# Kernel optimization log

Measured on AMD Instinct MI355X. Metric: run time of the kernel, lower is better.

## Reference

```python
import jax, jax.numpy as jnp
import numpy as np

B, T, C, H, W, NC = 128, 32, 512, 8, 32, 6625
HH = C // 2  # per-direction LSTM hidden


def setup_inputs() -> dict:
    key = jax.random.key(0)
    ks = jax.random.split(key, 20)
    u = lambda k, shape, n: jax.random.uniform(k, shape, jnp.float32, -1.0 / np.sqrt(n), 1.0 / np.sqrt(n))
    return dict(
        feature=jax.random.normal(ks[0], (B, C, H, W), jnp.float32),
        attention_map=jax.random.uniform(ks[1], (B, T, H, W), jnp.float32) + 1e-3,
        text=jax.random.randint(ks[2], (B, T), 0, NC),
        text_length=jnp.full((B,), T, dtype=jnp.int32),
        char_embeddings=jax.random.normal(ks[3], (NC, C), jnp.float32),
        lstm_w_ih_f=u(ks[4], (4 * HH, C), HH),
        lstm_w_hh_f=u(ks[5], (4 * HH, HH), HH),
        lstm_b_ih_f=u(ks[6], (4 * HH,), HH),
        lstm_b_hh_f=u(ks[7], (4 * HH,), HH),
        lstm_w_ih_b=u(ks[8], (4 * HH, C), HH),
        lstm_w_hh_b=u(ks[9], (4 * HH, HH), HH),
        lstm_b_ih_b=u(ks[10], (4 * HH,), HH),
        lstm_b_hh_b=u(ks[11], (4 * HH,), HH),
        gru_w_ih=u(ks[12], (3 * C, 2 * C), C),
        gru_w_hh=u(ks[13], (3 * C, C), C),
        gru_b_ih=u(ks[14], (3 * C,), C),
        gru_b_hh=u(ks[15], (3 * C,), C),
        gen_w=u(ks[16], (NC, C), C),
        gen_b=u(ks[17], (NC,), C),
    )


def _lstm_dir(xs, w_ih, w_hh, b_ih, b_hh):
    # xs: [T, B, C] -> hs: [T, B, HH]; PyTorch gate order i, f, g, o
    b = xs.shape[1]
    hh = w_hh.shape[1]
    def step(carry, xt):
        h, c = carry
        g = xt @ w_ih.T + h @ w_hh.T + (b_ih + b_hh)
        i, f, gg, o = jnp.split(g, 4, axis=-1)
        c = jax.nn.sigmoid(f) * c + jax.nn.sigmoid(i) * jnp.tanh(gg)
        h = jax.nn.sigmoid(o) * jnp.tanh(c)
        return (h, c), h
    h0 = jnp.zeros((b, hh), xs.dtype)
    _, hs = jax.lax.scan(step, (h0, h0), xs)
    return hs


def reference(feature, attention_map, text, text_length, char_embeddings,
              lstm_w_ih_f, lstm_w_hh_f, lstm_b_ih_f, lstm_b_hh_f,
              lstm_w_ih_b, lstm_w_hh_b, lstm_b_ih_b, lstm_b_hh_b,
              gru_w_ih, gru_w_hh, gru_b_ih, gru_b_hh, gen_w, gen_b):
    b, c, h, w = feature.shape
    t = attention_map.shape[1]
    # normalize attention over spatial dims, attention-pool features: [T, B, C]
    att = attention_map / attention_map.sum(axis=(2, 3), keepdims=True)
    cseq = jnp.einsum('bchw,bthw->tbc', feature, att)
    # bidirectional LSTM (dropout is identity in eval mode)
    hs_f = _lstm_dir(cseq, lstm_w_ih_f, lstm_w_hh_f, lstm_b_ih_f, lstm_b_hh_f)
    hs_b = _lstm_dir(cseq[::-1], lstm_w_ih_b, lstm_w_hh_b, lstm_b_ih_b, lstm_b_hh_b)[::-1]
    cseq = jnp.concatenate([hs_f, hs_b], axis=-1)  # [T, B, C]
    # teacher-forced previous-char embeddings: step 0 uses index 0
    prev_idx = jnp.concatenate([jnp.zeros((b, 1), text.dtype), text[:, :-1]], axis=1)  # [B, T]
    prev_emb = jnp.transpose(char_embeddings[prev_idx], (1, 0, 2))  # [T, B, C]
    # GRUCell decode; PyTorch gate order r, z, n
    def gru_step(hid, inp):
        ct, pe = inp
        x = jnp.concatenate([ct, pe], axis=-1)  # [B, 2C]
        gi = x @ gru_w_ih.T + gru_b_ih
        gh = hid @ gru_w_hh.T + gru_b_hh
        ir, iz, inn = jnp.split(gi, 3, axis=-1)
        hr, hz, hn = jnp.split(gh, 3, axis=-1)
        r = jax.nn.sigmoid(ir + hr)
        z = jax.nn.sigmoid(iz + hz)
        n = jnp.tanh(inn + r * hn)
        hid = (1.0 - z) * n + z * hid
        return hid, hid
    h0 = jnp.zeros((b, c), cseq.dtype)
    _, gru_res = jax.lax.scan(gru_step, h0, (cseq, prev_emb))  # [T, B, C]
    logits = gru_res @ gen_w.T + gen_b  # [T, B, NC]
    # pack per text_length; lengths are all == T so this equals a reshape
    out_res = jnp.transpose(logits, (1, 0, 2)).reshape(b * t, -1)
    out_attentions = att.reshape(b * t, h, w)
    return (out_res, out_attentions)
```

## Files before the change

kernel.cpp:

```cpp
#include <hip/hip_runtime.h>
#include <math.h>

typedef __attribute__((ext_vector_type(8))) short sh8;
typedef __attribute__((ext_vector_type(4))) short sh4;
typedef __attribute__((ext_vector_type(4))) float f4;
typedef __attribute__((ext_vector_type(4))) unsigned u4;

__device__ inline short f2bf(float f) {
    union { float f; unsigned u; } v; v.f = f;
    unsigned u = v.u;
    return (short)((u + 0x7fffu + ((u >> 16) & 1u)) >> 16);
}
__device__ inline sh8 as_sh8(u4 v) { union { u4 u; sh8 s; } c; c.u = v; return c.s; }

__device__ inline float sigm(float x)  { return __builtin_amdgcn_rcpf(1.f + __builtin_amdgcn_exp2f(-1.44269504f * x)); }
__device__ inline float tanha(float x) { return 1.f - 2.f * __builtin_amdgcn_rcpf(1.f + __builtin_amdgcn_exp2f(2.88539008f * x)); }

__device__ inline sh8 frag8(const float* __restrict__ p) {
    f4 a = *(const f4*)p;
    f4 b = *(const f4*)(p + 4);
    sh8 r;
    r[0]=f2bf(a[0]); r[1]=f2bf(a[1]); r[2]=f2bf(a[2]); r[3]=f2bf(a[3]);
    r[4]=f2bf(b[0]); r[5]=f2bf(b[1]); r[6]=f2bf(b[2]); r[7]=f2bf(b[3]);
    return r;
}

__device__ inline u4 cload_u4(const void* p) {
    u4 r;
    asm volatile("global_load_dwordx4 %0, %1, off sc0 sc1" : "=v"(r) : "v"(p));
    return r;
}

__device__ inline void grp_signal(int* myflag, int epoch) {
    asm volatile("s_waitcnt vmcnt(0)" ::: "memory");
    __builtin_amdgcn_sched_barrier(0);
    __syncthreads();
    if (threadIdx.x == 0)
        __hip_atomic_store(myflag, epoch, __ATOMIC_RELAXED, __HIP_MEMORY_SCOPE_AGENT);
}
__device__ inline void grp_wait(const int* fbase, int nb, int epoch) {
    if (threadIdx.x < 64) {
        int lane = threadIdx.x;
        bool need = lane < nb;
        const int* fp = fbase + lane * 16;
        while (true) {
            int v = need ? __hip_atomic_load(fp, __ATOMIC_RELAXED, __HIP_MEMORY_SCOPE_AGENT)
                         : 0x7fffffff;
            if (__ballot(need && (v < epoch)) == 0ull) break;
            __builtin_amdgcn_s_sleep(1);
        }
    }
    __syncthreads();
}

__global__ void zero_ctr(int* c, int n) {
    int i = blockIdx.x * blockDim.x + threadIdx.x;
    if (i < n) c[i] = 0;
}

struct CvtPack { const float* s[7]; short* d[7]; int n4[7]; };
__global__ void cvt_bf16(CvtPack p) {
    int job = blockIdx.y;
    const f4* s = (const f4*)p.s[job];
    sh4* d = (sh4*)p.d[job];
    int n4 = p.n4[job];
    for (int i = blockIdx.x * blockDim.x + threadIdx.x; i < n4; i += gridDim.x * blockDim.x) {
        f4 v = s[i];
        sh4 o; o[0]=f2bf(v[0]); o[1]=f2bf(v[1]); o[2]=f2bf(v[2]); o[3]=f2bf(v[3]);
        d[i] = o;
    }
}

__global__ void bias_prep(const float* bihf, const float* bhhf,
                          const float* bihb, const float* bhhb, float* biasL) {
    int n = blockIdx.x * blockDim.x + threadIdx.x;
    biasL[n] = (n < 1024) ? bihf[n] + bhhf[n] : bihb[n - 1024] + bhhb[n - 1024];
}

__global__ void att_norm(const float* __restrict__ att, float* __restrict__ outA) {
    int row = blockIdx.x;
    int tid = threadIdx.x;
    const float* p = att + (size_t)row * 256;
    f4 v = *(const f4*)(p + tid * 4);
    float sum = v[0] + v[1] + v[2] + v[3];
    #pragma unroll
    for (int off = 32; off; off >>= 1) sum += __shfl_down(sum, off);
    float inv = 1.f / __shfl(sum, 0);
    f4 o; o[0]=v[0]*inv; o[1]=v[1]*inv; o[2]=v[2]*inv; o[3]=v[3]*inv;
    *(f4*)(outA + (size_t)row * 256 + tid * 4) = o;
}

__global__ __launch_bounds__(256)
void pool_gemm(const float* __restrict__ feature, const float* __restrict__ att,
               short* __restrict__ cseqb) {
    int bz = blockIdx.y;
    const float* A  = feature + (size_t)bz * 512 * 256;
    const float* Wt = att + (size_t)bz * 32 * 256;
    int wave = threadIdx.x >> 6, lane = threadIdx.x & 63, r = lane & 15, hh = lane >> 4;
    int m0 = blockIdx.x * 64 + wave * 16;
    f4 acc[2] = {};
    const float* ar = A  + (size_t)(m0 + r) * 256 + hh * 8;
    const float* w0 = Wt + (size_t)r * 256 + hh * 8;
    const float* w1 = Wt + (size_t)(16 + r) * 256 + hh * 8;
    for (int kk = 0; kk < 256; kk += 32) {
        sh8 af = frag8(ar + kk);
        acc[0] = __builtin_amdgcn_mfma_f32_16x16x32_bf16(af, frag8(w0 + kk), acc[0], 0, 0, 0);
        acc[1] = __builtin_amdgcn_mfma_f32_16x16x32_bf16(af, frag8(w1 + kk), acc[1], 0, 0, 0);
    }
    #pragma unroll
    for (int j = 0; j < 2; j++) {
        int t = j * 16 + r;
        #pragma unroll
        for (int reg = 0; reg < 4; reg++) {
            int c = m0 + hh * 4 + reg;
            cseqb[(size_t)t * 65536 + (size_t)bz * 512 + c] = f2bf(acc[j][reg]);
        }
    }
}

template<int MODE>
__global__ __launch_bounds__(256)
void gemm128(const short* __restrict__ A, const short* __restrict__ W,
             const float* __restrict__ bias1, const float* __restrict__ bias2,
             float* __restrict__ out, int M, int N, int K) {
    __shared__ short lds[2][2][4096];
    const int tid = threadIdx.x, wave = tid >> 6, lane = tid & 63;
    const int r = lane & 15, hh = lane >> 4;
    const int wm = wave >> 1, wn = wave & 1;
    const int m0 = blockIdx.x * 128, n0 = blockIdx.y * 128;

    const int c0 = tid, c1 = 256 + tid;
    const int r0 = c0 >> 2, r1 = c1 >> 2;
    const int s0 = ((c0 & 3) ^ ((r0 >> 1) & 3));
    const int s1 = ((c1 & 3) ^ ((r1 >> 1) & 3));
    const short* gA0 = A + (size_t)(m0 + r0) * K + s0 * 8;
    const short* gA1 = A + (size_t)(m0 + r1) * K + s1 * 8;
    int wr0 = n0 + r0; if (wr0 > N - 1) wr0 = N - 1;
    int wr1 = n0 + r1; if (wr1 > N - 1) wr1 = N - 1;
    const short* gW0 = W + (size_t)wr0 * K + s0 * 8;
    const short* gW1 = W + (size_t)wr1 * K + s1 * 8;
    const int lo0 = (wave * 64) * 8, lo1 = (256 + wave * 64) * 8;

    auto stage = [&](int buf, int kt) {
        int ko = kt * 32;
        __builtin_amdgcn_global_load_lds((const __attribute__((address_space(1))) void*)(gA0 + ko),
            (__attribute__((address_space(3))) void*)&lds[buf][0][lo0], 16, 0, 0);
        __builtin_amdgcn_global_load_lds((const __attribute__((address_space(1))) void*)(gA1 + ko),
            (__attribute__((address_space(3))) void*)&lds[buf][0][lo1], 16, 0, 0);
        __builtin_amdgcn_global_load_lds((const __attribute__((address_space(1))) void*)(gW0 + ko),
            (__attribute__((address_space(3))) void*)&lds[buf][1][lo0], 16, 0, 0);
        __builtin_amdgcn_global_load_lds((const __attribute__((address_space(1))) void*)(gW1 + ko),
            (__attribute__((address_space(3))) void*)&lds[buf][1][lo1], 16, 0, 0);
    };

    f4 acc[4][4] = {};
    const int NT = K / 32;
    int cur = 0;

    stage(0, 0);
    __syncthreads();
    for (int kt = 0; kt < NT; ++kt) {
        if (kt + 1 < NT) stage(cur ^ 1, kt + 1);
        const char* As = (const char*)&lds[cur][0][0];
        const char* Ws = (const char*)&lds[cur][1][0];
        sh8 a[4], b[4];
        #pragma unroll
        for (int i = 0; i < 4; i++) {
            int row = wm * 64 + i * 16 + r;
            a[i] = *(const sh8*)(As + row * 64 + ((hh ^ ((row >> 1) & 3)) * 16));
        }
        #pragma unroll
        for (int i = 0; i < 4; i++) {
            int row = wn * 64 + i * 16 + r;
            b[i] = *(const sh8*)(Ws + row * 64 + ((hh ^ ((row >> 1) & 3)) * 16));
        }
        #pragma unroll
        for (int i = 0; i < 4; i++)
            #pragma unroll
            for (int j = 0; j < 4; j++)
                acc[i][j] = __builtin_amdgcn_mfma_f32_16x16x32_bf16(a[i], b[j], acc[i][j], 0, 0, 0);
        __syncthreads();
        cur ^= 1;
    }

    float bsj[4];
    #pragma unroll
    for (int j = 0; j < 4; j++) {
        int n = n0 + wn * 64 + j * 16 + r;
        int nc = n < N ? n : N - 1;
        bsj[j] = (bias1 ? bias1[nc] : 0.f) + (bias2 ? bias2[nc] : 0.f);
    }

    float* fl = (float*)&lds[0][0][0];
    #pragma unroll
    for (int hhalf = 0; hhalf < 2; hhalf++) {
        __syncthreads();
        if (wm == hhalf) {
            #pragma unroll
            for (int i = 0; i < 4; i++)
                #pragma unroll
                for (int j = 0; j < 4; j++) {
                    int col = wn * 64 + j * 16 + r;
                    #pragma unroll
                    for (int reg = 0; reg < 4; reg++)
                        fl[(i * 16 + hh * 4 + reg) * 128 + col] = acc[i][j][reg] + bsj[j];
                }
        }
        __syncthreads();
        #pragma unroll
        for (int it = 0; it < 8; it++) {
            int c = it * 256 + tid;
            int row = c >> 5, cf4 = c & 31;
            int n = n0 + cf4 * 4;
            int mrow = m0 + hhalf * 64 + row;
            size_t orow = (MODE == 0) ? (size_t)mrow
                                      : ((size_t)(mrow & 127) * 32 + (mrow >> 7));
            if (n + 3 < N) {
                *(f4*)&out[orow * N + n] = *(const f4*)&fl[row * 128 + cf4 * 4];
            } else {
                #pragma unroll
                for (int d = 0; d < 4; d++)
                    if (n + d < N) out[orow * N + n + d] = fl[row * 128 + cf4 * 4 + d];
            }
        }
    }
}

__global__ void emb_fill(const int* __restrict__ text, const float* __restrict__ emb,
                         short* __restrict__ xcatb) {
    int n = blockIdx.x;
    int t = n >> 7, b = n & 127;
    int idx = (t == 0) ? 0 : text[b * 32 + (t - 1)];
    const f4* src = (const f4*)(emb + (size_t)idx * 512);
    sh4* dst = (sh4*)(xcatb + (size_t)n * 1024 + 512);
    for (int j = threadIdx.x; j < 128; j += 64) {
        f4 v = src[j];
        sh4 o; o[0]=f2bf(v[0]); o[1]=f2bf(v[1]); o[2]=f2bf(v[2]); o[3]=f2bf(v[3]);
        dst[j] = o;
    }
}

__global__ __launch_bounds__(128)
void lstm_chain(const float* __restrict__ xfb,
                const short* __restrict__ whhf_b, const short* __restrict__ whhb_b,
                short* __restrict__ xcatb,
                int* __restrict__ flags) {
    extern __shared__ short wlds[];
    const int blk = blockIdx.x;
    const int dir = blk >> 5;
    const int mg  = (blk >> 2) & 7;
    const int ug  = blk & 3;
    const int m0 = mg * 16, u0 = ug * 64;
    const short* whh = dir ? whhb_b : whhf_b;
    const int dcol = dir ? 256 : 0;

    int* grp_flags = flags + (dir * 8 + mg) * 4 * 16;
    int* my_flag   = grp_flags + ug * 16;

    const int tid = threadIdx.x, w = tid >> 6, lane = tid & 63;
    const int r = lane & 15, hh = lane >> 4;
    unsigned* xcat32 = (unsigned*)xcatb;

    for (int i = 0; i < 64; i++) {
        int c = i * 128 + tid;
        int col = c >> 5, off = c & 31;
        int g = col >> 6, ul = col & 63;
        sh8 v = *(const sh8*)(whh + ((size_t)(g * 256 + u0 + ul)) * 256 + off * 8);
        *(sh8*)((char*)wlds + col * 512 + ((off * 16) ^ ((col & 7) << 4))) = v;
    }
    __syncthreads();

    const int mb = m0 + hh * 4;
    float c_state[2][4] = {};

    float xv[4][2][4];
    {
        const int t0 = dir ? 31 : 0;
        #pragma unroll
        for (int g = 0; g < 4; g++)
            #pragma unroll
            for (int j = 0; j < 2; j++)
                #pragma unroll
                for (int reg = 0; reg < 4; reg++)
                    xv[g][j][reg] = xfb[((size_t)t0 * 128 + mb + reg) * 2048 + dir * 1024
                                        + g * 256 + u0 + w * 32 + j * 16 + r];
    }

    for (int s = 0; s < 32; s++) {
        const int t = dir ? (31 - s) : s;
        f4 acc[4][2] = {};
        if (s > 0) {
            grp_wait(grp_flags, 4, s);
            const int tp = dir ? (t + 1) : (t - 1);
            const short* arow = xcatb + ((size_t)tp * 128 + m0 + r) * 1024 + dcol + hh * 8;
            u4 afr[8];
            #pragma unroll
            for (int kk = 0; kk < 8; kk++) afr[kk] = cload_u4(arow + kk * 32);
            asm volatile("s_waitcnt vmcnt(0)" ::: "memory");
            __builtin_amdgcn_sched_barrier(0);
            #pragma unroll
            for (int kk = 0; kk < 8; kk++) {
                sh8 af = as_sh8(afr[kk]);
                #pragma unroll
                for (int g = 0; g < 4; g++)
                    #pragma unroll
                    for (int j = 0; j < 2; j++) {
                        int colr = g * 64 + w * 32 + j * 16 + r;
                        sh8 bf = *(const sh8*)((const char*)wlds + colr * 512 +
                                  ((kk * 64 + hh * 16) ^ ((colr & 7) << 4)));
                        acc[g][j] = __builtin_amdgcn_mfma_f32_16x16x32_bf16(af, bf, acc[g][j], 0, 0, 0);
                    }
            }
        }
        #pragma unroll
        for (int j = 0; j < 2; j++)
            #pragma unroll
            for (int reg = 0; reg < 4; reg++) {
                int m = mb + reg;
                int u = u0 + w * 32 + j * 16 + r;
                float gI = acc[0][j][reg] + xv[0][j][reg];
                float gF = acc[1][j][reg] + xv[1][j][reg];
                float gG = acc[2][j][reg] + xv[2][j][reg];
                float gO = acc[3][j][reg] + xv[3][j][reg];
                float cn = sigm(gF) * c_state[j][reg] + sigm(gI) * tanha(gG);
                c_state[j][reg] = cn;
                float h = sigm(gO) * tanha(cn);
                unsigned hb = (unsigned)(unsigned short)f2bf(h);
                unsigned pb = (unsigned)__shfl_xor((int)hb, 1, 64);
                if (!(r & 1))
                    __hip_atomic_store(&xcat32[((size_t)t * 128 + m) * 512 + ((dcol + u) >> 1)],
                                       hb | (pb << 16), __ATOMIC_RELAXED, __HIP_MEMORY_SCOPE_AGENT);
            }
        if (s < 31) {
            grp_signal(my_flag, s + 1);
            const int tn = dir ? (t - 1) : (t + 1);
            #pragma unroll
            for (int g = 0; g < 4; g++)
                #pragma unroll
                for (int j = 0; j < 2; j++)
                    #pragma unroll
                    for (int reg = 0; reg < 4; reg++)
                        xv[g][j][reg] = xfb[((size_t)tn * 128 + mb + reg) * 2048 + dir * 1024
                                            + g * 256 + u0 + w * 32 + j * 16 + r];
        }
    }
}

__global__ __launch_bounds__(128)
void gru_chain(const float* __restrict__ gi,
               const short* __restrict__ gwhh_b, const float* __restrict__ bhh,
               short* __restrict__ gresb,
               int* __restrict__ flags) {
    extern __shared__ short wlds[];
    const int blk = blockIdx.x;
    const int mg = blk >> 4, ug = blk & 15;
    const int m0 = mg * 16, u0 = ug * 32;

    int* grp_flags = flags + mg * 16 * 16;
    int* my_flag   = grp_flags + ug * 16;

    const int tid = threadIdx.x, w = tid >> 6, lane = tid & 63;
    const int r = lane & 15, hh = lane >> 4;
    unsigned* gres32 = (unsigned*)gresb;

    for (int i = 0; i < 48; i++) {
        int c = i * 128 + tid;
        int col = c >> 6, off = c & 63;
        int g = col >> 5, ul = col & 31;
        sh8 v = *(const sh8*)(gwhh_b + ((size_t)(g * 512 + u0 + ul)) * 512 + off * 8);
        *(sh8*)((char*)wlds + col * 1024 + ((off * 16) ^ ((col & 7) << 4))) = v;
    }
    __syncthreads();

    const int mb = m0 + hh * 4;
    const int u = u0 + w * 16 + r;
    const float bh_r = bhh[u], bh_z = bhh[512 + u], bh_n = bhh[1024 + u];
    float h_state[4] = {0.f, 0.f, 0.f, 0.f};

    float gv[3][4];
    #pragma unroll
    for (int g = 0; g < 3; g++)
        #pragma unroll
        for (int reg = 0; reg < 4; reg++)
            gv[g][reg] = gi[((size_t)(mb + reg)) * 1536 + g * 512 + u];

    for (int t = 0; t < 32; t++) {
        f4 acc[3] = {};
        if (t > 0) {
            grp_wait(grp_flags, 16, t);
            const short* arow = gresb + ((size_t)(t - 1) * 128 + m0 + r) * 512 + hh * 8;
            u4 afr[16];
            #pragma unroll
            for (int kk = 0; kk < 16; kk++) afr[kk] = cload_u4(arow + kk * 32);
            asm volatile("s_waitcnt vmcnt(0)" ::: "memory");
            __builtin_amdgcn_sched_barrier(0);
            #pragma unroll
            for (int kk = 0; kk < 16; kk++) {
                sh8 af = as_sh8(afr[kk]);
                #pragma unroll
                for (int g = 0; g < 3; g++) {
                    int colr = g * 32 + w * 16 + r;
                    sh8 bf = *(const sh8*)((const char*)wlds + colr * 1024 +
                              ((kk * 64 + hh * 16) ^ ((colr & 7) << 4)));
                    acc[g] = __builtin_amdgcn_mfma_f32_16x16x32_bf16(af, bf, acc[g], 0, 0, 0);
                }
            }
        }
        #pragma unroll
        for (int reg = 0; reg < 4; reg++) {
            int m = mb + reg;
            float rr = sigm(gv[0][reg] + acc[0][reg] + bh_r);
            float zz = sigm(gv[1][reg] + acc[1][reg] + bh_z);
            float nn = tanha(gv[2][reg] + rr * (acc[2][reg] + bh_n));
            float h = (1.f - zz) * nn + zz * h_state[reg];
            h_state[reg] = h;
            unsigned hb = (unsigned)(unsigned short)f2bf(h);
            unsigned pb = (unsigned)__shfl_xor((int)hb, 1, 64);
            if (!(r & 1))
                __hip_atomic_store(&gres32[((size_t)t * 128 + m) * 256 + (u >> 1)],
                                   hb | (pb << 16), __ATOMIC_RELAXED, __HIP_MEMORY_SCOPE_AGENT);
        }
        if (t < 31) {
            grp_signal(my_flag, t + 1);
            #pragma unroll
            for (int g = 0; g < 3; g++)
                #pragma unroll
                for (int reg = 0; reg < 4; reg++)
                    gv[g][reg] = gi[((size_t)(t + 1) * 128 + mb + reg) * 1536 + g * 512 + u];
        }
    }
}

extern "C" void kernel_launch(void* const* d_in, const int* in_sizes, int n_in,
                              void* d_out, int out_size, void* d_ws, size_t ws_size,
                              hipStream_t stream) {
    const float* feature = (const float*)d_in[0];
    const float* attmap  = (const float*)d_in[1];
    const int*   text    = (const int*)d_in[2];
    const float* cemb    = (const float*)d_in[4];
    const float* wihf    = (const float*)d_in[5];
    const float* whhf    = (const float*)d_in[6];
    const float* bihf    = (const float*)d_in[7];
    const float* bhhf    = (const float*)d_in[8];
    const float* wihb    = (const float*)d_in[9];
    const float* whhb    = (const float*)d_in[10];
    const float* bihb    = (const float*)d_in[11];
    const float* bhhb    = (const float*)d_in[12];
    const float* gwih    = (const float*)d_in[13];
    const float* gwhh    = (const float*)d_in[14];
    const float* gbih    = (const float*)d_in[15];
    const float* gbhh    = (const float*)d_in[16];
    const float* genw    = (const float*)d_in[17];
    const float* genb    = (const float*)d_in[18];

    float* out    = (float*)d_out;
    float* outAtt = out + (size_t)4096 * 6625;

    float* xfb   = (float*)d_ws;
    float* gi    = xfb + 8388608;
    float* biasL = gi + 6291456;
    int*   flags = (int*)(biasL + 2048);
    short* cseqb  = (short*)(flags + 4096);
    short* xcatb  = cseqb + 2097152;
    short* gresb  = xcatb + 4194304;
    short* wih_b  = gresb + 2097152;
    short* whhf_b = wih_b + 1048576;
    short* whhb_b = whhf_b + 262144;
    short* gwih_b = whhb_b + 262144;
    short* gwhh_b = gwih_b + 1572864;
    short* genw_b = gwhh_b + 786432;

    hipFuncSetAttribute((const void*)lstm_chain,
                        hipFuncAttributeMaxDynamicSharedMemorySize, 131072);
    hipFuncSetAttribute((const void*)gru_chain,
                        hipFuncAttributeMaxDynamicSharedMemorySize, 98304);

    zero_ctr<<<dim3(16), dim3(256), 0, stream>>>(flags, 4096);

    CvtPack p;
    p.s[0] = wihf; p.d[0] = wih_b;           p.n4[0] = 524288 / 4;
    p.s[1] = wihb; p.d[1] = wih_b + 524288;  p.n4[1] = 524288 / 4;
    p.s[2] = whhf; p.d[2] = whhf_b;          p.n4[2] = 262144 / 4;
    p.s[3] = whhb; p.d[3] = whhb_b;          p.n4[3] = 262144 / 4;
    p.s[4] = gwih; p.d[4] = gwih_b;          p.n4[4] = 1572864 / 4;
    p.s[5] = gwhh; p.d[5] = gwhh_b;          p.n4[5] = 786432 / 4;
    p.s[6] = genw; p.d[6] = genw_b;          p.n4[6] = 3392000 / 4;
    cvt_bf16<<<dim3(128, 7), dim3(256), 0, stream>>>(p);
    bias_prep<<<dim3(8), dim3(256), 0, stream>>>(bihf, bhhf, bihb, bhhb, biasL);

    att_norm<<<dim3(4096), dim3(64), 0, stream>>>(attmap, outAtt);
    pool_gemm<<<dim3(8, 128), dim3(256), 0, stream>>>(feature, outAtt, cseqb);

    gemm128<0><<<dim3(32, 16), dim3(256), 0, stream>>>(cseqb, wih_b, biasL, nullptr,
                                                       xfb, 4096, 2048, 512);
    emb_fill<<<dim3(4096), dim3(64), 0, stream>>>(text, cemb, xcatb);

    lstm_chain<<<dim3(64), dim3(128), 131072, stream>>>(xfb, whhf_b, whhb_b, xcatb, flags);

    gemm128<0><<<dim3(32, 12), dim3(256), 0, stream>>>(xcatb, gwih_b, gbih, nullptr,
                                                       gi, 4096, 1536, 1024);

    gru_chain<<<dim3(128), dim3(128), 98304, stream>>>(gi, gwhh_b, gbhh, gresb, flags + 1024);

    gemm128<1><<<dim3(32, 52), dim3(256), 0, stream>>>(gresb, genw_b, genb, nullptr,
                                                       out, 4096, 6625, 512);
}
```

Measured before the change: 420.0 us.

## Run each LSTM batch slice in one 1024-thread block with register-resident weights

The LSTM recurrence kernel no longer splits hidden units across 64 small blocks that coordinate through global flag spin-waits. Each of 16 blocks now owns a 16-row batch slice with all 256 units for one direction. The recurrent weights live in registers, and the new hidden state is passed between waves through a double-buffered, swizzled LDS tile with one __syncthreads per step. This removes the cross-block global synchronisation and the global reload of h each step, at the cost of far fewer active CUs, heavy register pressure (128 VGPRs of weights per thread under a 1024-thread launch bound, with spill risk), and unprefetched per-step xfb loads.

After: 582.0 us. +38.6%, slower.

```diff
diff --git a/kernel.cpp b/kernel.cpp
--- a/kernel.cpp
+++ b/kernel.cpp
@@ -240,108 +240,67 @@
     }
 }
 
-__global__ __launch_bounds__(128)
+__global__ __launch_bounds__(1024)
 void lstm_chain(const float* __restrict__ xfb,
                 const short* __restrict__ whhf_b, const short* __restrict__ whhb_b,
-                short* __restrict__ xcatb,
-                int* __restrict__ flags) {
-    extern __shared__ short wlds[];
+                short* __restrict__ xcatb) {
+    __shared__ short hbuf[2][16 * 256];
     const int blk = blockIdx.x;
-    const int dir = blk >> 5;
-    const int mg  = (blk >> 2) & 7;
-    const int ug  = blk & 3;
-    const int m0 = mg * 16, u0 = ug * 64;
+    const int dir = blk >> 3;
+    const int m0  = (blk & 7) * 16;
     const short* whh = dir ? whhb_b : whhf_b;
     const int dcol = dir ? 256 : 0;
 
-    int* grp_flags = flags + (dir * 8 + mg) * 4 * 16;
-    int* my_flag   = grp_flags + ug * 16;
-
-    const int tid = threadIdx.x, w = tid >> 6, lane = tid & 63;
+    const int tid = threadIdx.x, w4 = tid >> 6, lane = tid & 63;
     const int r = lane & 15, hh = lane >> 4;
-    unsigned* xcat32 = (unsigned*)xcatb;
-
-    for (int i = 0; i < 64; i++) {
-        int c = i * 128 + tid;
-        int col = c >> 5, off = c & 31;
-        int g = col >> 6, ul = col & 63;
-        sh8 v = *(const sh8*)(whh + ((size_t)(g * 256 + u0 + ul)) * 256 + off * 8);
-        *(sh8*)((char*)wlds + col * 512 + ((off * 16) ^ ((col & 7) << 4))) = v;
-    }
-    __syncthreads();
-
-    const int mb = m0 + hh * 4;
-    float c_state[2][4] = {};
-
-    float xv[4][2][4];
-    {
-        const int t0 = dir ? 31 : 0;
-        #pragma unroll
-        for (int g = 0; g < 4; g++)
-            #pragma unroll
-            for (int j = 0; j < 2; j++)
-                #pragma unroll
-                for (int reg = 0; reg < 4; reg++)
-                    xv[g][j][reg] = xfb[((size_t)t0 * 128 + mb + reg) * 2048 + dir * 1024
-                                        + g * 256 + u0 + w * 32 + j * 16 + r];
-    }
+    const int u = w4 * 16 + r;
+
+    sh8 breg[4][8];
+    #pragma unroll
+    for (int g = 0; g < 4; g++) {
+        const short* wrow = whh + ((size_t)(g * 256 + u)) * 256 + hh * 8;
+        #pragma unroll
+        for (int kk = 0; kk < 8; kk++) breg[g][kk] = *(const sh8*)(wrow + kk * 32);
+    }
+
+    float c_state[4] = {0.f, 0.f, 0.f, 0.f};
 
     for (int s = 0; s < 32; s++) {
         const int t = dir ? (31 - s) : s;
-        f4 acc[4][2] = {};
+        float xv[4][4];
+        #pragma unroll
+        for (int g = 0; g < 4; g++)
+            #pragma unroll
+            for (int reg = 0; reg < 4; reg++)
+                xv[g][reg] = xfb[((size_t)t * 128 + m0 + hh * 4 + reg) * 2048
+                                 + dir * 1024 + g * 256 + u];
+        f4 acc[4] = {};
         if (s > 0) {
-            grp_wait(grp_flags, 4, s);
-            const int tp = dir ? (t + 1) : (t - 1);
-            const short* arow = xcatb + ((size_t)tp * 128 + m0 + r) * 1024 + dcol + hh * 8;
-            u4 afr[8];
-            #pragma unroll
-            for (int kk = 0; kk < 8; kk++) afr[kk] = cload_u4(arow + kk * 32);
-            asm volatile("s_waitcnt vmcnt(0)" ::: "memory");
-            __builtin_amdgcn_sched_barrier(0);
+            __syncthreads();
+            const char* hb = (const char*)&hbuf[(s - 1) & 1][0];
             #pragma unroll
             for (int kk = 0; kk < 8; kk++) {
-                sh8 af = as_sh8(afr[kk]);
+                sh8 af = *(const sh8*)(hb + r * 512 +
+                          ((kk * 64 + hh * 16) ^ ((r & 7) << 4)));
                 #pragma unroll
                 for (int g = 0; g < 4; g++)
-                    #pragma unroll
-                    for (int j = 0; j < 2; j++) {
-                        int colr = g * 64 + w * 32 + j * 16 + r;
-                        sh8 bf = *(const sh8*)((const char*)wlds + colr * 512 +
-                                  ((kk * 64 + hh * 16) ^ ((colr & 7) << 4)));
-                        acc[g][j] = __builtin_amdgcn_mfma_f32_16x16x32_bf16(af, bf, acc[g][j], 0, 0, 0);
-                    }
+                    acc[g] = __builtin_amdgcn_mfma_f32_16x16x32_bf16(af, breg[g][kk], acc[g], 0, 0, 0);
             }
         }
-        #pragma unroll
-        for (int j = 0; j < 2; j++)
-            #pragma unroll
-            for (int reg = 0; reg < 4; reg++) {
-                int m = mb + reg;
-                int u = u0 + w * 32 + j * 16 + r;
-                float gI = acc[0][j][reg] + xv[0][j][reg];
-                float gF = acc[1][j][reg] + xv[1][j][reg];
-                float gG = acc[2][j][reg] + xv[2][j][reg];
-                float gO = acc[3][j][reg] + xv[3][j][reg];
-                float cn = sigm(gF) * c_state[j][reg] + sigm(gI) * tanha(gG);
-                c_state[j][reg] = cn;
-                float h = sigm(gO) * tanha(cn);
-                unsigned hb = (unsigned)(unsigned short)f2bf(h);
-                unsigned pb = (unsigned)__shfl_xor((int)hb, 1, 64);
-                if (!(r & 1))
-                    __hip_atomic_store(&xcat32[((size_t)t * 128 + m) * 512 + ((dcol + u) >> 1)],
-                                       hb | (pb << 16), __ATOMIC_RELAXED, __HIP_MEMORY_SCOPE_AGENT);
-            }
-        if (s < 31) {
-            grp_signal(my_flag, s + 1);
-            const int tn = dir ? (t - 1) : (t + 1);
-            #pragma unroll
-            for (int g = 0; g < 4; g++)
-                #pragma unroll
-                for (int j = 0; j < 2; j++)
-                    #pragma unroll
-                    for (int reg = 0; reg < 4; reg++)
-                        xv[g][j][reg] = xfb[((size_t)tn * 128 + mb + reg) * 2048 + dir * 1024
-                                            + g * 256 + u0 + w * 32 + j * 16 + r];
+        char* hw = (char*)&hbuf[s & 1][0];
+        #pragma unroll
+        for (int reg = 0; reg < 4; reg++) {
+            int row = hh * 4 + reg;
+            float gI = acc[0][reg] + xv[0][reg];
+            float gF = acc[1][reg] + xv[1][reg];
+            float gG = acc[2][reg] + xv[2][reg];
+            float gO = acc[3][reg] + xv[3][reg];
+            float cn = sigm(gF) * c_state[reg] + sigm(gI) * tanha(gG);
+            c_state[reg] = cn;
+            float h = sigm(gO) * tanha(cn);
+            short hbv = f2bf(h);
+            xcatb[((size_t)t * 128 + m0 + row) * 1024 + dcol + u] = hbv;
+            *(short*)(hw + row * 512 + ((u * 2) ^ ((row & 7) << 4))) = hbv;
         }
     }
 }
@@ -470,8 +429,6 @@
     short* gwhh_b = gwih_b + 1572864;
     short* genw_b = gwhh_b + 786432;
 
-    hipFuncSetAttribute((const void*)lstm_chain,
-                        hipFuncAttributeMaxDynamicSharedMemorySize, 131072);
     hipFuncSetAttribute((const void*)gru_chain,
                         hipFuncAttributeMaxDynamicSharedMemorySize, 98304);
 
@@ -495,12 +452,12 @@
                                                        xfb, 4096, 2048, 512);
     emb_fill<<<dim3(4096), dim3(64), 0, stream>>>(text, cemb, xcatb);
 
-    lstm_chain<<<dim3(64), dim3(128), 131072, stream>>>(xfb, whhf_b, whhb_b, xcatb, flags);
+    lstm_chain<<<dim3(16), dim3(1024), 0, stream>>>(xfb, whhf_b, whhb_b, xcatb);
 
     gemm128<0><<<dim3(32, 12), dim3(256), 0, stream>>>(xcatb, gwih_b, gbih, nullptr,
                                                        gi, 4096, 1536, 1024);
 
-    gru_chain<<<dim3(128), dim3(128), 98304, stream>>>(gi, gwhh_b, gbhh, gresb, flags + 1024);
+    gru_chain<<<dim3(128), dim3(128), 98304, stream>>>(gi, gwhh_b, gbhh, gresb, flags);
 
     gemm128<1><<<dim3(32, 52), dim3(256), 0, stream>>>(gresb, genw_b, genb, nullptr,
                                                        out, 4096, 6625, 512);
```

## Interleave two independent recurrence chains per block in LSTM and GRU kernels

Applied to the files above, without the earlier changes.

Each LSTM block now processes both forward and backward directions for a narrower unit slice, keeping both weight sets in LDS. Each GRU block now handles two batch groups in alternation, which halves the grid. While one chain waits on its cross-block flags, the block can do useful work on the other chain, hiding some synchronization latency. The cost is more blocks per sync group (8 instead of 4 for the LSTM), more LDS per LSTM block, and fewer blocks overall. The flag offset for the GRU is also moved so its flags do not overlap the LSTM's.

After: 548.2 us. 30.5% more time.

```diff
diff --git a/kernel.cpp b/kernel.cpp
--- a/kernel.cpp
+++ b/kernel.cpp
@@ -247,101 +247,140 @@
                 int* __restrict__ flags) {
     extern __shared__ short wlds[];
     const int blk = blockIdx.x;
-    const int dir = blk >> 5;
-    const int mg  = (blk >> 2) & 7;
-    const int ug  = blk & 3;
-    const int m0 = mg * 16, u0 = ug * 64;
-    const short* whh = dir ? whhb_b : whhf_b;
-    const int dcol = dir ? 256 : 0;
-
-    int* grp_flags = flags + (dir * 8 + mg) * 4 * 16;
-    int* my_flag   = grp_flags + ug * 16;
+    const int mg = blk >> 3, ug = blk & 7;
+    const int m0 = mg * 16, u0 = ug * 32;
+
+    int* gfF = flags + (0 * 8 + mg) * 128;
+    int* gfB = flags + (1 * 8 + mg) * 128;
+    int* myF = gfF + ug * 16;
+    int* myB = gfB + ug * 16;
 
     const int tid = threadIdx.x, w = tid >> 6, lane = tid & 63;
     const int r = lane & 15, hh = lane >> 4;
     unsigned* xcat32 = (unsigned*)xcatb;
 
-    for (int i = 0; i < 64; i++) {
-        int c = i * 128 + tid;
-        int col = c >> 5, off = c & 31;
-        int g = col >> 6, ul = col & 63;
-        sh8 v = *(const sh8*)(whh + ((size_t)(g * 256 + u0 + ul)) * 256 + off * 8);
-        *(sh8*)((char*)wlds + col * 512 + ((off * 16) ^ ((col & 7) << 4))) = v;
+    #pragma unroll
+    for (int d = 0; d < 2; d++) {
+        const short* whh = d ? whhb_b : whhf_b;
+        for (int i = 0; i < 32; i++) {
+            int c = i * 128 + tid;
+            int col = c >> 5, off = c & 31;
+            int g = col >> 5, ul = col & 31;
+            sh8 v = *(const sh8*)(whh + ((size_t)(g * 256 + u0 + ul)) * 256 + off * 8);
+            *(sh8*)((char*)wlds + d * 65536 + col * 512 + ((off * 16) ^ ((col & 7) << 4))) = v;
+        }
     }
     __syncthreads();
 
     const int mb = m0 + hh * 4;
-    float c_state[2][4] = {};
-
-    float xv[4][2][4];
-    {
-        const int t0 = dir ? 31 : 0;
-        #pragma unroll
-        for (int g = 0; g < 4; g++)
-            #pragma unroll
-            for (int j = 0; j < 2; j++)
-                #pragma unroll
-                for (int reg = 0; reg < 4; reg++)
-                    xv[g][j][reg] = xfb[((size_t)t0 * 128 + mb + reg) * 2048 + dir * 1024
-                                        + g * 256 + u0 + w * 32 + j * 16 + r];
-    }
+    const int u = u0 + w * 16 + r;
+    float c_f[4] = {}, c_b[4] = {};
+
+    float xvF[4][4], xvB[4][4];
+    #pragma unroll
+    for (int g = 0; g < 4; g++)
+        #pragma unroll
+        for (int reg = 0; reg < 4; reg++) {
+            xvF[g][reg] = xfb[((size_t)0 * 128 + mb + reg) * 2048 + 0 + g * 256 + u];
+            xvB[g][reg] = xfb[((size_t)31 * 128 + mb + reg) * 2048 + 1024 + g * 256 + u];
+        }
 
     for (int s = 0; s < 32; s++) {
-        const int t = dir ? (31 - s) : s;
-        f4 acc[4][2] = {};
-        if (s > 0) {
-            grp_wait(grp_flags, 4, s);
-            const int tp = dir ? (t + 1) : (t - 1);
-            const short* arow = xcatb + ((size_t)tp * 128 + m0 + r) * 1024 + dcol + hh * 8;
-            u4 afr[8];
-            #pragma unroll
-            for (int kk = 0; kk < 8; kk++) afr[kk] = cload_u4(arow + kk * 32);
-            asm volatile("s_waitcnt vmcnt(0)" ::: "memory");
-            __builtin_amdgcn_sched_barrier(0);
-            #pragma unroll
-            for (int kk = 0; kk < 8; kk++) {
-                sh8 af = as_sh8(afr[kk]);
-                #pragma unroll
-                for (int g = 0; g < 4; g++)
-                    #pragma unroll
-                    for (int j = 0; j < 2; j++) {
-                        int colr = g * 64 + w * 32 + j * 16 + r;
+        {
+            const int t = s;
+            f4 acc[4] = {};
+            if (s > 0) {
+                grp_wait(gfF, 8, s);
+                const short* arow = xcatb + ((size_t)(t - 1) * 128 + m0 + r) * 1024 + 0 + hh * 8;
+                u4 afr[8];
+                #pragma unroll
+                for (int kk = 0; kk < 8; kk++) afr[kk] = cload_u4(arow + kk * 32);
+                asm volatile("s_waitcnt vmcnt(0)" ::: "memory");
+                __builtin_amdgcn_sched_barrier(0);
+                #pragma unroll
+                for (int kk = 0; kk < 8; kk++) {
+                    sh8 af = as_sh8(afr[kk]);
+                    #pragma unroll
+                    for (int g = 0; g < 4; g++) {
+                        int colr = g * 32 + w * 16 + r;
                         sh8 bf = *(const sh8*)((const char*)wlds + colr * 512 +
                                   ((kk * 64 + hh * 16) ^ ((colr & 7) << 4)));
-                        acc[g][j] = __builtin_amdgcn_mfma_f32_16x16x32_bf16(af, bf, acc[g][j], 0, 0, 0);
+                        acc[g] = __builtin_amdgcn_mfma_f32_16x16x32_bf16(af, bf, acc[g], 0, 0, 0);
                     }
-            }
-        }
-        #pragma unroll
-        for (int j = 0; j < 2; j++)
+                }
+            }
             #pragma unroll
             for (int reg = 0; reg < 4; reg++) {
                 int m = mb + reg;
-                int u = u0 + w * 32 + j * 16 + r;
-                float gI = acc[0][j][reg] + xv[0][j][reg];
-                float gF = acc[1][j][reg] + xv[1][j][reg];
-                float gG = acc[2][j][reg] + xv[2][j][reg];
-                float gO = acc[3][j][reg] + xv[3][j][reg];
-                float cn = sigm(gF) * c_state[j][reg] + sigm(gI) * tanha(gG);
-                c_state[j][reg] = cn;
+                float gI = acc[0][reg] + xvF[0][reg];
+                float gF = acc[1][reg] + xvF[1][reg];
+                float gG = acc[2][reg] + xvF[2][reg];
+                float gO = acc[3][reg] + xvF[3][reg];
+                float cn = sigm(gF) * c_f[reg] + sigm(gI) * tanha(gG);
+                c_f[reg] = cn;
                 float h = sigm(gO) * tanha(cn);
                 unsigned hb = (unsigned)(unsigned short)f2bf(h);
                 unsigned pb = (unsigned)__shfl_xor((int)hb, 1, 64);
                 if (!(r & 1))
-                    __hip_atomic_store(&xcat32[((size_t)t * 128 + m) * 512 + ((dcol + u) >> 1)],
+                    __hip_atomic_store(&xcat32[((size_t)t * 128 + m) * 512 + (u >> 1)],
                                        hb | (pb << 16), __ATOMIC_RELAXED, __HIP_MEMORY_SCOPE_AGENT);
             }
-        if (s < 31) {
-            grp_signal(my_flag, s + 1);
-            const int tn = dir ? (t - 1) : (t + 1);
+            if (s < 31) {
+                grp_signal(myF, s + 1);
+                #pragma unroll
+                for (int g = 0; g < 4; g++)
+                    #pragma unroll
+                    for (int reg = 0; reg < 4; reg++)
+                        xvF[g][reg] = xfb[((size_t)(t + 1) * 128 + mb + reg) * 2048 + g * 256 + u];
+            }
+        }
+        {
+            const int t = 31 - s;
+            f4 acc[4] = {};
+            if (s > 0) {
+                grp_wait(gfB, 8, s);
+                const short* arow = xcatb + ((size_t)(t + 1) * 128 + m0 + r) * 1024 + 256 + hh * 8;
+                u4 afr[8];
+                #pragma unroll
+                for (int kk = 0; kk < 8; kk++) afr[kk] = cload_u4(arow + kk * 32);
+                asm volatile("s_waitcnt vmcnt(0)" ::: "memory");
+                __builtin_amdgcn_sched_barrier(0);
+                #pragma unroll
+                for (int kk = 0; kk < 8; kk++) {
+                    sh8 af = as_sh8(afr[kk]);
+                    #pragma unroll
+                    for (int g = 0; g < 4; g++) {
+                        int colr = g * 32 + w * 16 + r;
+                        sh8 bf = *(const sh8*)((const char*)wlds + 65536 + colr * 512 +
+                                  ((kk * 64 + hh * 16) ^ ((colr & 7) << 4)));
+                        acc[g] = __builtin_amdgcn_mfma_f32_16x16x32_bf16(af, bf, acc[g], 0, 0, 0);
+                    }
+                }
+            }
             #pragma unroll
-            for (int g = 0; g < 4; g++)
-                #pragma unroll
-                for (int j = 0; j < 2; j++)
+            for (int reg = 0; reg < 4; reg++) {
+                int m = mb + reg;
+                float gI = acc[0][reg] + xvB[0][reg];
+                float gF = acc[1][reg] + xvB[1][reg];
+                float gG = acc[2][reg] + xvB[2][reg];
+                float gO = acc[3][reg] + xvB[3][reg];
+                float cn = sigm(gF) * c_b[reg] + sigm(gI) * tanha(gG);
+                c_b[reg] = cn;
+                float h = sigm(gO) * tanha(cn);
+                unsigned hb = (unsigned)(unsigned short)f2bf(h);
+                unsigned pb = (unsigned)__shfl_xor((int)hb, 1, 64);
+                if (!(r & 1))
+                    __hip_atomic_store(&xcat32[((size_t)t * 128 + m) * 512 + 128 + (u >> 1)],
+                                       hb | (pb << 16), __ATOMIC_RELAXED, __HIP_MEMORY_SCOPE_AGENT);
+            }
+            if (s < 31) {
+                grp_signal(myB, s + 1);
+                #pragma unroll
+                for (int g = 0; g < 4; g++)
                     #pragma unroll
                     for (int reg = 0; reg < 4; reg++)
-                        xv[g][j][reg] = xfb[((size_t)tn * 128 + mb + reg) * 2048 + dir * 1024
-                                            + g * 256 + u0 + w * 32 + j * 16 + r];
+                        xvB[g][reg] = xfb[((size_t)(t - 1) * 128 + mb + reg) * 2048 + 1024 + g * 256 + u];
+            }
         }
     }
 }
@@ -353,11 +392,14 @@
                int* __restrict__ flags) {
     extern __shared__ short wlds[];
     const int blk = blockIdx.x;
-    const int mg = blk >> 4, ug = blk & 15;
-    const int m0 = mg * 16, u0 = ug * 32;
-
-    int* grp_flags = flags + mg * 16 * 16;
-    int* my_flag   = grp_flags + ug * 16;
+    const int p = blk >> 4, ug = blk & 15;
+    const int m0A = p * 16, m0B = (p + 4) * 16;
+    const int u0 = ug * 32;
+
+    int* gfA = flags + p * 256;
+    int* gfB = flags + (p + 4) * 256;
+    int* myA = gfA + ug * 16;
+    int* myB = gfB + ug * 16;
 
     const int tid = threadIdx.x, w = tid >> 6, lane = tid & 63;
     const int r = lane & 15, hh = lane >> 4;
@@ -372,61 +414,110 @@
     }
     __syncthreads();
 
-    const int mb = m0 + hh * 4;
+    const int mbA = m0A + hh * 4, mbB = m0B + hh * 4;
     const int u = u0 + w * 16 + r;
     const float bh_r = bhh[u], bh_z = bhh[512 + u], bh_n = bhh[1024 + u];
-    float h_state[4] = {0.f, 0.f, 0.f, 0.f};
-
-    float gv[3][4];
+    float hA[4] = {}, hB[4] = {};
+
+    float gvA[3][4], gvB[3][4];
     #pragma unroll
     for (int g = 0; g < 3; g++)
         #pragma unroll
-        for (int reg = 0; reg < 4; reg++)
-            gv[g][reg] = gi[((size_t)(mb + reg)) * 1536 + g * 512 + u];
+        for (int reg = 0; reg < 4; reg++) {
+            gvA[g][reg] = gi[((size_t)(mbA + reg)) * 1536 + g * 512 + u];
+            gvB[g][reg] = gi[((size_t)(mbB + reg)) * 1536 + g * 512 + u];
+        }
 
     for (int t = 0; t < 32; t++) {
-        f4 acc[3] = {};
-        if (t > 0) {
-            grp_wait(grp_flags, 16, t);
-            const short* arow = gresb + ((size_t)(t - 1) * 128 + m0 + r) * 512 + hh * 8;
-            u4 afr[16];
+        {
+            f4 acc[3] = {};
+            if (t > 0) {
+                grp_wait(gfA, 16, t);
+                const short* arow = gresb + ((size_t)(t - 1) * 128 + m0A + r) * 512 + hh * 8;
+                u4 afr[16];
+                #pragma unroll
+                for (int kk = 0; kk < 16; kk++) afr[kk] = cload_u4(arow + kk * 32);
+                asm volatile("s_waitcnt vmcnt(0)" ::: "memory");
+                __builtin_amdgcn_sched_barrier(0);
+                #pragma unroll
+                for (int kk = 0; kk < 16; kk++) {
+                    sh8 af = as_sh8(afr[kk]);
+                    #pragma unroll
+                    for (int g = 0; g < 3; g++) {
+                        int colr = g * 32 + w * 16 + r;
+                        sh8 bf = *(const sh8*)((const char*)wlds + colr * 1024 +
+                                  ((kk * 64 + hh * 16) ^ ((colr & 7) << 4)));
+                        acc[g] = __builtin_amdgcn_mfma_f32_16x16x32_bf16(af, bf, acc[g], 0, 0, 0);
+                    }
+                }
+            }
             #pragma unroll
-            for (int kk = 0; kk < 16; kk++) afr[kk] = cload_u4(arow + kk * 32);
-            asm volatile("s_waitcnt vmcnt(0)" ::: "memory");
-            __builtin_amdgcn_sched_barrier(0);
+            for (int reg = 0; reg < 4; reg++) {
+                int m = mbA + reg;
+                float rr = sigm(gvA[0][reg] + acc[0][reg] + bh_r);
+                float zz = sigm(gvA[1][reg] + acc[1][reg] + bh_z);
+                float nn = tanha(gvA[2][reg] + rr * (acc[2][reg] + bh_n));
+                float h = (1.f - zz) * nn + zz * hA[reg];
+                hA[reg] = h;
+                unsigned hb = (unsigned)(unsigned short)f2bf(h);
+                unsigned pb = (unsigned)__shfl_xor((int)hb, 1, 64);
+                if (!(r & 1))
+                    __hip_atomic_store(&gres32[((size_t)t * 128 + m) * 256 + (u >> 1)],
+                                       hb | (pb << 16), __ATOMIC_RELAXED, __HIP_MEMORY_SCOPE_AGENT);
+            }
+            if (t < 31) {
+                grp_signal(myA, t + 1);
+                #pragma unroll
+                for (int g = 0; g < 3; g++)
+                    #pragma unroll
+                    for (int reg = 0; reg < 4; reg++)
+                        gvA[g][reg] = gi[((size_t)(t + 1) * 128 + mbA + reg) * 1536 + g * 512 + u];
+            }
+        }
+        {
+            f4 acc[3] = {};
+            if (t > 0) {
+                grp_wait(gfB, 16, t);
+                const short* arow = gresb + ((size_t)(t - 1) * 128 + m0B + r) * 512 + hh * 8;
+                u4 afr[16];
+                #pragma unroll
+                for (int kk = 0; kk < 16; kk++) afr[kk] = cload_u4(arow + kk * 32);
+                asm volatile("s_waitcnt vmcnt(0)" ::: "memory");
+                __builtin_amdgcn_sched_barrier(0);
+                #pragma unroll
+                for (int kk = 0; kk < 16; kk++) {
+                    sh8 af = as_sh8(afr[kk]);
+                    #pragma unroll
+                    for (int g = 0; g < 3; g++) {
+                        int colr = g * 32 + w * 16 + r;
+                        sh8 bf = *(const sh8*)((const char*)wlds + colr * 1024 +
+                                  ((kk * 64 + hh * 16) ^ ((colr & 7) << 4)));
+                        acc[g] = __builtin_amdgcn_mfma_f32_16x16x32_bf16(af, bf, acc[g], 0, 0, 0);
+                    }
+                }
+            }
             #pragma unroll
-            for (int kk = 0; kk < 16; kk++) {
-                sh8 af = as_sh8(afr[kk]);
-                #pragma unroll
-                for (int g = 0; g < 3; g++) {
-                    int colr = g * 32 + w * 16 + r;
-                    sh8 bf = *(const sh8*)((const char*)wlds + colr * 1024 +
-                              ((kk * 64 + hh * 16) ^ ((colr & 7) << 4)));
-                    acc[g] = __builtin_amdgcn_mfma_f32_16x16x32_bf16(af, bf, acc[g], 0, 0, 0);
-                }
-            }
-        }
-        #pragma unroll
-        for (int reg = 0; reg < 4; reg++) {
-            int m = mb + reg;
-            float rr = sigm(gv[0][reg] + acc[0][reg] + bh_r);
-            float zz = sigm(gv[1][reg] + acc[1][reg] + bh_z);
-            float nn = tanha(gv[2][reg] + rr * (acc[2][reg] + bh_n));
-            float h = (1.f - zz) * nn + zz * h_state[reg];
-            h_state[reg] = h;
-            unsigned hb = (unsigned)(unsigned short)f2bf(h);
-            unsigned pb = (unsigned)__shfl_xor((int)hb, 1, 64);
-            if (!(r & 1))
-                __hip_atomic_store(&gres32[((size_t)t * 128 + m) * 256 + (u >> 1)],
-                                   hb | (pb << 16), __ATOMIC_RELAXED, __HIP_MEMORY_SCOPE_AGENT);
-        }
-        if (t < 31) {
-            grp_signal(my_flag, t + 1);
-            #pragma unroll
-            for (int g = 0; g < 3; g++)
-                #pragma unroll
-                for (int reg = 0; reg < 4; reg++)
-                    gv[g][reg] = gi[((size_t)(t + 1) * 128 + mb + reg) * 1536 + g * 512 + u];
+            for (int reg = 0; reg < 4; reg++) {
+                int m = mbB + reg;
+                float rr = sigm(gvB[0][reg] + acc[0][reg] + bh_r);
+                float zz = sigm(gvB[1][reg] + acc[1][reg] + bh_z);
+                float nn = tanha(gvB[2][reg] + rr * (acc[2][reg] + bh_n));
+                float h = (1.f - zz) * nn + zz * hB[reg];
+                hB[reg] = h;
+                unsigned hb = (unsigned)(unsigned short)f2bf(h);
+                unsigned pb = (unsigned)__shfl_xor((int)hb, 1, 64);
+                if (!(r & 1))
+                    __hip_atomic_store(&gres32[((size_t)t * 128 + m) * 256 + (u >> 1)],
+                                       hb | (pb << 16), __ATOMIC_RELAXED, __HIP_MEMORY_SCOPE_AGENT);
+            }
+            if (t < 31) {
+                grp_signal(myB, t + 1);
+                #pragma unroll
+                for (int g = 0; g < 3; g++)
+                    #pragma unroll
+                    for (int reg = 0; reg < 4; reg++)
+                        gvB[g][reg] = gi[((size_t)(t + 1) * 128 + mbB + reg) * 1536 + g * 512 + u];
+            }
         }
     }
 }
@@ -500,7 +591,7 @@
     gemm128<0><<<dim3(32, 12), dim3(256), 0, stream>>>(xcatb, gwih_b, gbih, nullptr,
                                                        gi, 4096, 1536, 1024);
 
-    gru_chain<<<dim3(128), dim3(128), 98304, stream>>>(gi, gwhh_b, gbhh, gresb, flags + 1024);
+    gru_chain<<<dim3(64), dim3(128), 98304, stream>>>(gi, gwhh_b, gbhh, gresb, flags + 2048);
 
     gemm128<1><<<dim3(32, 52), dim3(256), 0, stream>>>(gresb, genw_b, genb, nullptr,
                                                        out, 4096, 6625, 512);
```
